# Kernel tuning notes

Hardware: AMD Instinct MI355X
Metric: run time of the kernel (lower is better)

## Reference

```python
import jax, jax.numpy as jnp
import numpy as np
import math

HEAD = 4
B, N, C = 8, 1024, 256


def setup_inputs() -> dict:
    key = jax.random.key(0)
    k1, k2, k3, k4, k5 = jax.random.split(key, 5)
    query = jax.random.normal(k1, (B, N, C), dtype=jnp.float32)
    keyt = jax.random.normal(k2, (B, N, C), dtype=jnp.float32)
    value = jax.random.normal(k3, (B, N, C), dtype=jnp.float32)
    mask = jax.random.randint(k4, (B, N, N), 0, 2).astype(bool)
    dis = jax.random.normal(k5, (B, N, N), dtype=jnp.float32)
    return {"query": query, "key": keyt, "value": value, "mask": mask, "dis": dis}


def reference(query, key, value, mask, dis):
    Bq, Nq, Cq = key.shape
    d = Cq // HEAD
    # split heads: [B,N,C] -> [h,B,N,d]
    q = query.reshape(Bq, Nq, HEAD, d).transpose(2, 0, 1, 3)
    k = key.reshape(Bq, Nq, HEAD, d).transpose(2, 0, 1, 3)
    v = value.reshape(Bq, Nq, HEAD, d).transpose(2, 0, 1, 3)
    # scores: [h,B,N,N]; note: dis added BEFORE scaling, as in the torch code
    scores = jnp.einsum('hbnd,hbmd->hbnm', q, k)
    scores = scores + dis[None]            # dis broadcasts over head dim
    scores = scores / math.sqrt(d)
    scores = jnp.where(mask[None], -jnp.inf, scores)
    p_attn = jax.nn.softmax(scores, axis=-1)
    out = jnp.einsum('hbnm,hbmd->hbnd', p_attn, v)  # [h,B,N,d]
    out = out.transpose(1, 2, 0, 3).reshape(Bq, Nq, Cq)
    return out, p_attn
```

## Files before the change

kernel.cpp:

```cpp
#include <hip/hip_runtime.h>
#include <math.h>

#define HEADS 4
#define BATCH 8
#define SEQ   1024
#define CH    256
#define DH    64
#define RB    16
#define NTHR  512
#define SSTR  1032

typedef float  floatx4  __attribute__((ext_vector_type(4)));
typedef float  floatx2  __attribute__((ext_vector_type(2)));
typedef short  shortx8  __attribute__((ext_vector_type(8)));

__device__ __forceinline__ unsigned short f2bf(float f) {
    unsigned u = __float_as_uint(f);
    unsigned r = u + 0x7FFFu + ((u >> 16) & 1u);
    return (unsigned short)(r >> 16);
}
__device__ __forceinline__ float bf2f(unsigned short h) {
    return __uint_as_float(((unsigned)h) << 16);
}
__device__ __forceinline__ shortx8 pack8(float4 a, float4 b) {
    shortx8 r;
    r[0] = (short)f2bf(a.x); r[1] = (short)f2bf(a.y);
    r[2] = (short)f2bf(a.z); r[3] = (short)f2bf(a.w);
    r[4] = (short)f2bf(b.x); r[5] = (short)f2bf(b.y);
    r[6] = (short)f2bf(b.z); r[7] = (short)f2bf(b.w);
    return r;
}

__global__ __launch_bounds__(256)
void prep(const float* __restrict__ q, const float* __restrict__ k,
          const float* __restrict__ v, unsigned short* __restrict__ qb,
          unsigned short* __restrict__ kb, unsigned short* __restrict__ vt)
{
    const int t = threadIdx.x;
    const int bid = blockIdx.x;
    if (bid < 2048) {
        const float* src = (bid < 1024) ? q : k;
        unsigned short* dst = (bid < 1024) ? qb : kb;
        size_t idx = (size_t)(bid & 1023) * 2048 + (size_t)t * 8;
        float4 a = *(const float4*)(src + idx);
        float4 b = *(const float4*)(src + idx + 4);
        *(shortx8*)(dst + idx) = pack8(a, b);
        return;
    }
    __shared__ unsigned short tl[64][68];
    const int vb = bid - 2048;
    const int nt = vb & 15, h = (vb >> 4) & 3, b = vb >> 6;
    const int n0 = nt * 64;
    const float* vsrc = v + ((size_t)(b * SEQ + n0)) * CH + h * DH;
    #pragma unroll
    for (int it = 0; it < 4; ++it) {
        int fid = it * 256 + t;
        int n = fid >> 4, cc = (fid & 15) * 4;
        float4 x = *(const float4*)(vsrc + (size_t)n * CH + cc);
        tl[n][cc]     = f2bf(x.x);
        tl[n][cc + 1] = f2bf(x.y);
        tl[n][cc + 2] = f2bf(x.z);
        tl[n][cc + 3] = f2bf(x.w);
    }
    __syncthreads();
    unsigned short* vout = vt + ((size_t)((b * HEADS + h) * DH)) * SEQ + n0;
    #pragma unroll
    for (int it = 0; it < 2; ++it) {
        int cid = it * 256 + t;
        int d = cid >> 3, nc = cid & 7;
        shortx8 r;
        #pragma unroll
        for (int j = 0; j < 8; ++j) r[j] = (short)tl[nc * 8 + j][d];
        *(shortx8*)(vout + (size_t)d * SEQ + nc * 8) = r;
    }
}

__global__ __launch_bounds__(NTHR, 8)
void attn_mfma(const unsigned short* __restrict__ qb,
               const unsigned short* __restrict__ kbf,
               const unsigned short* __restrict__ vt,
               const void* __restrict__ maskp,
               const float* __restrict__ dis, float* __restrict__ out,
               float* __restrict__ pout)
{
    __shared__ unsigned short Sraw[RB][SSTR];
    __shared__ float Opart[RB][65];
    __shared__ float invs[RB];

    const int t   = threadIdx.x;
    const int bid = blockIdx.x;
    const int b   = bid & (BATCH - 1);
    const int h   = (bid >> 3) & (HEADS - 1);
    const int n0  = (bid >> 5) * RB;

    const int lane = t & 63;
    const int w    = t >> 6;
    const int ln   = lane & 15;
    const int qd   = lane >> 4;

    int fl;
    {
        const unsigned* mw = (const unsigned*)maskp;
        int found = 0;
        #pragma unroll
        for (int j = 0; j < 16; ++j)
            if (mw[lane * 16 + j] & 0xFFFFFF00u) found = 1;
        fl = (__ballot(found != 0) != 0ULL) ? 1 : 0;
    }
    const unsigned char* mask8  = (const unsigned char*)maskp;
    const int*           mask32 = (const int*)maskp;

    const unsigned short* qrow = qb + ((size_t)(b * SEQ + n0 + ln)) * CH + h * DH;
    shortx8 aq0 = *(const shortx8*)(qrow + qd * 8);
    shortx8 aq1 = *(const shortx8*)(qrow + 32 + qd * 8);

    const unsigned short* kbase = kbf + ((size_t)(b * SEQ)) * CH + h * DH;
    const unsigned short* vbase = vt + ((size_t)((b * HEADS + h) * DH)) * SEQ;

    #pragma unroll 2
    for (int mc = 0; mc < 8; ++mc) {
        const int mg = mc * 128 + w * 16 + ln;
        const size_t dibase = ((size_t)(b * SEQ + n0 + qd * 4)) * SEQ + mg;
        float dv[4]; int mk[4];
        #pragma unroll
        for (int r = 0; r < 4; ++r) dv[r] = dis[dibase + (size_t)r * SEQ];
        if (fl) {
            #pragma unroll
            for (int r = 0; r < 4; ++r) mk[r] = mask8[dibase + (size_t)r * SEQ];
        } else {
            #pragma unroll
            for (int r = 0; r < 4; ++r) mk[r] = mask32[dibase + (size_t)r * SEQ];
        }
        const unsigned short* krow = kbase + (size_t)mg * CH;
        shortx8 b0 = *(const shortx8*)(krow + qd * 8);
        shortx8 b1 = *(const shortx8*)(krow + 32 + qd * 8);
        floatx4 acc = {0.f, 0.f, 0.f, 0.f};
        acc = __builtin_amdgcn_mfma_f32_16x16x32_bf16(aq0, b0, acc, 0, 0, 0);
        acc = __builtin_amdgcn_mfma_f32_16x16x32_bf16(aq1, b1, acc, 0, 0, 0);
        #pragma unroll
        for (int r = 0; r < 4; ++r) {
            float sc = mk[r] ? -INFINITY : (acc[r] + dv[r]) * 0.125f;
            Sraw[qd * 4 + r][mg] = f2bf(sc);
        }
    }
    __syncthreads();

    {
        const int r = t >> 5, l = t & 31;
        float mx = -INFINITY;
        #pragma unroll
        for (int j = 0; j < 4; ++j) {
            shortx8 sv = *(const shortx8*)&Sraw[r][j * 256 + l * 8];
            #pragma unroll
            for (int e = 0; e < 8; ++e) mx = fmaxf(mx, bf2f((unsigned short)sv[e]));
        }
        #pragma unroll
        for (int off = 16; off; off >>= 1) mx = fmaxf(mx, __shfl_xor(mx, off, 32));
        float sum = 0.f;
        #pragma unroll
        for (int j = 0; j < 4; ++j) {
            shortx8 sv = *(const shortx8*)&Sraw[r][j * 256 + l * 8];
            shortx8 ev;
            #pragma unroll
            for (int e = 0; e < 8; ++e) {
                float x = __expf(bf2f((unsigned short)sv[e]) - mx);
                sum += x;
                ev[e] = (short)f2bf(x);
            }
            *(shortx8*)&Sraw[r][j * 256 + l * 8] = ev;
        }
        #pragma unroll
        for (int off = 16; off; off >>= 1) sum += __shfl_xor(sum, off, 32);
        if (l == 0) invs[r] = 1.0f / sum;
    }
    __syncthreads();

    {
        float* prow = pout + ((size_t)((h * BATCH + b) * SEQ + n0)) * SEQ;
        #pragma unroll
        for (int i = 0; i < RB; ++i) {
            const float inv = invs[i];
            unsigned pk = *(const unsigned*)&Sraw[i][t * 2];
            floatx2 pv = { bf2f((unsigned short)(pk & 0xFFFFu)) * inv,
                           bf2f((unsigned short)(pk >> 16)) * inv };
            __builtin_nontemporal_store(
                pv, (floatx2*)(prow + (size_t)i * SEQ + t * 2));
        }
    }

    const int hm = w >> 2;
    const int c  = (w & 3) * 16;
    floatx4 acco = {0.f, 0.f, 0.f, 0.f};
    const unsigned short* vcol = vbase + (size_t)(c + ln) * SEQ;
    #pragma unroll 2
    for (int mc = 0; mc < 8; ++mc) {
        #pragma unroll
        for (int s = 0; s < 2; ++s) {
            const int kk = hm * 512 + mc * 64 + s * 32 + qd * 8;
            shortx8 af  = *(const shortx8*)&Sraw[ln][kk];
            shortx8 bfv = *(const shortx8*)(vcol + kk);
            acco = __builtin_amdgcn_mfma_f32_16x16x32_bf16(af, bfv, acco, 0, 0, 0);
        }
    }
    if (hm == 1) {
        #pragma unroll
        for (int r = 0; r < 4; ++r) Opart[qd * 4 + r][c + ln] = acco[r];
    }
    __syncthreads();
    if (hm == 0) {
        #pragma unroll
        for (int r = 0; r < 4; ++r) {
            int row = qd * 4 + r;
            float ov = (acco[r] + Opart[row][c + ln]) * invs[row];
            __builtin_nontemporal_store(
                ov, out + ((size_t)(b * SEQ + n0 + row)) * CH + h * DH + c + ln);
        }
    }
}

extern "C" void kernel_launch(void* const* d_in, const int* in_sizes, int n_in,
                              void* d_out, int out_size, void* d_ws, size_t ws_size,
                              hipStream_t stream) {
    const float* q    = (const float*)d_in[0];
    const float* k    = (const float*)d_in[1];
    const float* v    = (const float*)d_in[2];
    const void*  mask = d_in[3];
    const float* dis  = (const float*)d_in[4];
    float* out  = (float*)d_out;
    float* pout = out + (size_t)BATCH * SEQ * CH;

    unsigned short* qb  = (unsigned short*)d_ws;
    unsigned short* kbw = qb  + (size_t)BATCH * SEQ * CH;
    unsigned short* vtw = kbw + (size_t)BATCH * SEQ * CH;
    (void)ws_size;

    prep<<<2560, 256, 0, stream>>>(q, k, v, qb, kbw, vtw);
    attn_mfma<<<HEADS * BATCH * (SEQ / RB), NTHR, 0, stream>>>(
        qb, kbw, vtw, mask, dis, out, pout);
}
```

Baseline: 286.1 us.

## Pack mask into bitmask in prep, preload dis into registers, reorder PV before P store

The prep kernel gains extra blocks that read the boolean mask once and pack 32 mask bits per word, so the attention kernel loads a single word per lane instead of re-reading the byte mask for every head. The attention kernel also preloads all 32 dis values into registers before the QK loop, moves the P·V MFMA loop ahead of the p_attn global store, and lowers the occupancy hint from 8 to 6. The aim is to cut mask traffic by a factor of the head count and to overlap latency better. The cost is an extra workspace buffer, more register pressure, and extra work in prep.

```diff
diff --git a/kernel.cpp b/kernel.cpp
--- a/kernel.cpp
+++ b/kernel.cpp
@@ -33,9 +33,11 @@
 
 __global__ __launch_bounds__(256)
 void prep(const float* __restrict__ q, const float* __restrict__ k,
-          const float* __restrict__ v, unsigned short* __restrict__ qb,
-          unsigned short* __restrict__ kb, unsigned short* __restrict__ vt)
+          const float* __restrict__ v, const void* __restrict__ maskp,
+          unsigned short* __restrict__ qb, unsigned short* __restrict__ kb,
+          unsigned short* __restrict__ vt, unsigned* __restrict__ pm)
 {
+    __shared__ unsigned short tl[64][68];
     const int t = threadIdx.x;
     const int bid = blockIdx.x;
     if (bid < 2048) {
@@ -47,39 +49,68 @@
         *(shortx8*)(dst + idx) = pack8(a, b);
         return;
     }
-    __shared__ unsigned short tl[64][68];
-    const int vb = bid - 2048;
-    const int nt = vb & 15, h = (vb >> 4) & 3, b = vb >> 6;
-    const int n0 = nt * 64;
-    const float* vsrc = v + ((size_t)(b * SEQ + n0)) * CH + h * DH;
+    if (bid < 2560) {
+        const int vb = bid - 2048;
+        const int nt = vb & 15, h = (vb >> 4) & 3, b = vb >> 6;
+        const int n0 = nt * 64;
+        const float* vsrc = v + ((size_t)(b * SEQ + n0)) * CH + h * DH;
+        #pragma unroll
+        for (int it = 0; it < 4; ++it) {
+            int fid = it * 256 + t;
+            int n = fid >> 4, cc = (fid & 15) * 4;
+            float4 x = *(const float4*)(vsrc + (size_t)n * CH + cc);
+            tl[n][cc]     = f2bf(x.x);
+            tl[n][cc + 1] = f2bf(x.y);
+            tl[n][cc + 2] = f2bf(x.z);
+            tl[n][cc + 3] = f2bf(x.w);
+        }
+        __syncthreads();
+        unsigned short* vout = vt + ((size_t)((b * HEADS + h) * DH)) * SEQ + n0;
+        #pragma unroll
+        for (int it = 0; it < 2; ++it) {
+            int cid = it * 256 + t;
+            int d = cid >> 3, nc = cid & 7;
+            shortx8 r;
+            #pragma unroll
+            for (int j = 0; j < 8; ++j) r[j] = (short)tl[nc * 8 + j][d];
+            *(shortx8*)(vout + (size_t)d * SEQ + nc * 8) = r;
+        }
+        return;
+    }
+    const int vb2 = bid - 2560;
+    const int b = vb2 >> 7, row8 = vb2 & 127;
+    const int sub = t >> 7, c0 = t & 127;
+    const int row4 = row8 * 2 + sub;
+    int fl;
+    {
+        const unsigned* mw = (const unsigned*)maskp;
+        const int lane = t & 63;
+        int found = 0;
+        #pragma unroll
+        for (int j = 0; j < 16; ++j)
+            if (mw[lane * 16 + j] & 0xFFFFFF00u) found = 1;
+        fl = (__ballot(found != 0) != 0ULL) ? 1 : 0;
+    }
+    const unsigned char* m8  = (const unsigned char*)maskp;
+    const int*           m32 = (const int*)maskp;
+    unsigned u = 0;
     #pragma unroll
-    for (int it = 0; it < 4; ++it) {
-        int fid = it * 256 + t;
-        int n = fid >> 4, cc = (fid & 15) * 4;
-        float4 x = *(const float4*)(vsrc + (size_t)n * CH + cc);
-        tl[n][cc]     = f2bf(x.x);
-        tl[n][cc + 1] = f2bf(x.y);
-        tl[n][cc + 2] = f2bf(x.z);
-        tl[n][cc + 3] = f2bf(x.w);
-    }
-    __syncthreads();
-    unsigned short* vout = vt + ((size_t)((b * HEADS + h) * DH)) * SEQ + n0;
-    #pragma unroll
-    for (int it = 0; it < 2; ++it) {
-        int cid = it * 256 + t;
-        int d = cid >> 3, nc = cid & 7;
-        shortx8 r;
-        #pragma unroll
-        for (int j = 0; j < 8; ++j) r[j] = (short)tl[nc * 8 + j][d];
-        *(shortx8*)(vout + (size_t)d * SEQ + nc * 8) = r;
-    }
-}
-
-__global__ __launch_bounds__(NTHR, 8)
+    for (int r = 0; r < 4; ++r) {
+        #pragma unroll
+        for (int mc = 0; mc < 8; ++mc) {
+            size_t idx = ((size_t)(b * SEQ + row4 * 4 + r)) * SEQ + mc * 128 + c0;
+            int mk = fl ? (int)m8[idx] : m32[idx];
+            u |= (mk ? 1u : 0u) << (r * 8 + mc);
+        }
+    }
+    pm[((b * 256 + row4) * 128) + c0] = u;
+}
+
+__global__ __launch_bounds__(NTHR, 6)
 void attn_mfma(const unsigned short* __restrict__ qb,
                const unsigned short* __restrict__ kbf,
                const unsigned short* __restrict__ vt,
-               const void* __restrict__ maskp,
+               const unsigned* __restrict__ pm,
                const float* __restrict__ dis, float* __restrict__ out,
                float* __restrict__ pout)
 {
@@ -98,17 +129,17 @@
     const int ln   = lane & 15;
     const int qd   = lane >> 4;
 
-    int fl;
-    {
-        const unsigned* mw = (const unsigned*)maskp;
-        int found = 0;
-        #pragma unroll
-        for (int j = 0; j < 16; ++j)
-            if (mw[lane * 16 + j] & 0xFFFFFF00u) found = 1;
-        fl = (__ballot(found != 0) != 0ULL) ? 1 : 0;
-    }
-    const unsigned char* mask8  = (const unsigned char*)maskp;
-    const int*           mask32 = (const int*)maskp;
+    float dreg[32];
+    {
+        const size_t dib0 = ((size_t)(b * SEQ + n0 + qd * 4)) * SEQ + w * 16 + ln;
+        #pragma unroll
+        for (int mc = 0; mc < 8; ++mc) {
+            #pragma unroll
+            for (int r = 0; r < 4; ++r)
+                dreg[mc * 4 + r] = dis[dib0 + (size_t)r * SEQ + mc * 128];
+        }
+    }
+    const unsigned mb = pm[((b * 256 + (n0 >> 2) + qd) * 128) + w * 16 + ln];
 
     const unsigned short* qrow = qb + ((size_t)(b * SEQ + n0 + ln)) * CH + h * DH;
     shortx8 aq0 = *(const shortx8*)(qrow + qd * 8);
@@ -120,17 +151,6 @@
     #pragma unroll 2
     for (int mc = 0; mc < 8; ++mc) {
         const int mg = mc * 128 + w * 16 + ln;
-        const size_t dibase = ((size_t)(b * SEQ + n0 + qd * 4)) * SEQ + mg;
-        float dv[4]; int mk[4];
-        #pragma unroll
-        for (int r = 0; r < 4; ++r) dv[r] = dis[dibase + (size_t)r * SEQ];
-        if (fl) {
-            #pragma unroll
-            for (int r = 0; r < 4; ++r) mk[r] = mask8[dibase + (size_t)r * SEQ];
-        } else {
-            #pragma unroll
-            for (int r = 0; r < 4; ++r) mk[r] = mask32[dibase + (size_t)r * SEQ];
-        }
         const unsigned short* krow = kbase + (size_t)mg * CH;
         shortx8 b0 = *(const shortx8*)(krow + qd * 8);
         shortx8 b1 = *(const shortx8*)(krow + 32 + qd * 8);
@@ -139,7 +159,9 @@
         acc = __builtin_amdgcn_mfma_f32_16x16x32_bf16(aq1, b1, acc, 0, 0, 0);
         #pragma unroll
         for (int r = 0; r < 4; ++r) {
-            float sc = mk[r] ? -INFINITY : (acc[r] + dv[r]) * 0.125f;
+            float sc = ((mb >> (r * 8 + mc)) & 1u)
+                           ? -INFINITY
+                           : (acc[r] + dreg[mc * 4 + r]) * 0.125f;
             Sraw[qd * 4 + r][mg] = f2bf(sc);
         }
     }
@@ -174,6 +196,18 @@
         if (l == 0) invs[r] = 1.0f / sum;
     }
     __syncthreads();
+
+    const int hm = w >> 2;
+    const int c  = (w & 3) * 16;
+    floatx4 acco = {0.f, 0.f, 0.f, 0.f};
+    const unsigned short* vcol = vbase + (size_t)(c + ln) * SEQ;
+    #pragma unroll 4
+    for (int it = 0; it < 16; ++it) {
+        const int kk = hm * 512 + (it >> 1) * 64 + (it & 1) * 32 + qd * 8;
+        shortx8 af  = *(const shortx8*)&Sraw[ln][kk];
+        shortx8 bfv = *(const shortx8*)(vcol + kk);
+        acco = __builtin_amdgcn_mfma_f32_16x16x32_bf16(af, bfv, acco, 0, 0, 0);
+    }
 
     {
         float* prow = pout + ((size_t)((h * BATCH + b) * SEQ + n0)) * SEQ;
@@ -188,20 +222,6 @@
         }
     }
 
-    const int hm = w >> 2;
-    const int c  = (w & 3) * 16;
-    floatx4 acco = {0.f, 0.f, 0.f, 0.f};
-    const unsigned short* vcol = vbase + (size_t)(c + ln) * SEQ;
-    #pragma unroll 2
-    for (int mc = 0; mc < 8; ++mc) {
-        #pragma unroll
-        for (int s = 0; s < 2; ++s) {
-            const int kk = hm * 512 + mc * 64 + s * 32 + qd * 8;
-            shortx8 af  = *(const shortx8*)&Sraw[ln][kk];
-            shortx8 bfv = *(const shortx8*)(vcol + kk);
-            acco = __builtin_amdgcn_mfma_f32_16x16x32_bf16(af, bfv, acco, 0, 0, 0);
-        }
-    }
     if (hm == 1) {
         #pragma unroll
         for (int r = 0; r < 4; ++r) Opart[qd * 4 + r][c + ln] = acco[r];
@@ -232,9 +252,10 @@
     unsigned short* qb  = (unsigned short*)d_ws;
     unsigned short* kbw = qb  + (size_t)BATCH * SEQ * CH;
     unsigned short* vtw = kbw + (size_t)BATCH * SEQ * CH;
+    unsigned*       pmw = (unsigned*)(vtw + (size_t)BATCH * SEQ * CH);
     (void)ws_size;
 
-    prep<<<2560, 256, 0, stream>>>(q, k, v, qb, kbw, vtw);
+    prep<<<3584, 256, 0, stream>>>(q, k, v, mask, qb, kbw, vtw, pmw);
     attn_mfma<<<HEADS * BATCH * (SEQ / RB), NTHR, 0, stream>>>(
-        qb, kbw, vtw, mask, dis, out, pout);
-}
+        qb, kbw, vtw, pmw, dis, out, pout);
+}
```

Result: slower. 321.0 us (+12.2%).
